# Performance work log

Measured on AMD Instinct MI355X. Metric: run time of the kernel, lower is better.

## Reference

```python
import jax, jax.numpy as jnp
import numpy as np

D_MODEL = 1024
NUM_HEADS = 16

def setup_inputs() -> dict:
    key = jax.random.key(0)
    ks = jax.random.split(key, 5)
    std = np.sqrt(2.0 / (D_MODEL + D_MODEL))
    def w(k):
        # trunc_normal approx: normal clipped to +-3 std
        v = jax.random.truncated_normal(k, -3.0, 3.0, (D_MODEL, D_MODEL), dtype=jnp.float32) * std
        return v
    return {
        "x": jax.random.normal(ks[0], (2, 2048, D_MODEL), dtype=jnp.float32),
        "w_q": w(ks[1]),
        "w_k": w(ks[2]),
        "w_v": w(ks[3]),
        "w_o": w(ks[4]),
    }

def reference(x, w_q, w_k, w_v, w_o):
    B, S, D = x.shape
    H = NUM_HEADS
    dk = D // H
    # Linear: y = x @ W^T  (weight is [d_out, d_in])
    def proj(w):
        y = jnp.einsum('bsd,ed->bse', x, w)
        return y.reshape(B, S, H, dk).transpose(0, 2, 1, 3)  # [B,H,S,dk]
    q, k, v = proj(w_q), proj(w_k), proj(w_v)
    scale = 1.0 / jnp.sqrt(jnp.float32(dk))
    scores = jnp.einsum('bhqd,bhkd->bhqk', q, k) * scale  # [B,H,S,S]
    causal = jnp.tril(jnp.ones((S, S), dtype=bool))
    scores = jnp.where(causal, scores, -jnp.inf)
    attn = jax.nn.softmax(scores, axis=-1)
    out = jnp.einsum('bhqk,bhkd->bhqd', attn, v)  # [B,H,S,dk]
    out = out.transpose(0, 2, 1, 3).reshape(B, S, D)
    return jnp.einsum('bsd,ed->bse', out, w_o)
```

## Files before the change

### kernel.cpp

```cpp
#include <hip/hip_runtime.h>
#include <hip/hip_bf16.h>
#include <stdint.h>

#define S_LEN 2048
#define DM    1024
#define NH    16
#define DK    64
#define NBATCH 2

typedef __attribute__((ext_vector_type(8))) short bf8_t;
typedef __attribute__((ext_vector_type(4))) short s4_t;
typedef __attribute__((ext_vector_type(4))) float f4_t;

using bf16 = __hip_bfloat16;

#define NEG_BIG (-1.0e30f)
#define SCALE2  (0.125f * 1.44269504088896f)

static __device__ __forceinline__ f4_t mfma16(bf8_t a, bf8_t b, f4_t c) {
    return __builtin_amdgcn_mfma_f32_16x16x32_bf16(a, b, c, 0, 0, 0);
}

static __device__ __forceinline__ short f2b(float f) {
    __hip_bfloat16 h = __float2bfloat16(f);
    return *reinterpret_cast<short*>(&h);
}

__global__ __launch_bounds__(256)
void gemm_qkv(const float* __restrict__ x,
              const float* __restrict__ wqp, const float* __restrict__ wkp,
              const float* __restrict__ wvp,
              bf16* __restrict__ qws, bf16* __restrict__ kws,
              bf16* __restrict__ vtws) {
    constexpr int K = DM;
    constexpr int BM = 128, BK = 32, LDT = BK + 8;

    const int z = blockIdx.z;
    const float* W = (z == 0) ? wqp : (z == 1) ? wkp : wvp;

    __shared__ bf16 As[BM][LDT];
    __shared__ bf16 Bs[BM][LDT];

    const int tid  = threadIdx.x;
    const int lane = tid & 63;
    const int w    = tid >> 6;
    const int wr   = w >> 1, wc = w & 1;
    const int lhi  = lane >> 4, llo = lane & 15;
    const int bm   = blockIdx.x * BM;
    const int bn   = blockIdx.y * BM;

    f4_t acc[4][4] = {};

    for (int k0 = 0; k0 < K; k0 += BK) {
        __syncthreads();
        #pragma unroll
        for (int t = 0; t < 2; ++t) {
            int c   = t * 256 + tid;
            int row = c >> 2;
            int col = (c & 3) << 3;
            {
                const float* s0 = x + (size_t)(bm + row) * K + k0 + col;
                float4 f0 = *(const float4*)(s0);
                float4 f1 = *(const float4*)(s0 + 4);
                bf8_t a8;
                a8[0]=f2b(f0.x); a8[1]=f2b(f0.y); a8[2]=f2b(f0.z); a8[3]=f2b(f0.w);
                a8[4]=f2b(f1.x); a8[5]=f2b(f1.y); a8[6]=f2b(f1.z); a8[7]=f2b(f1.w);
                *(bf8_t*)(&As[row][col]) = a8;
            }
            {
                const float* s0 = W + (size_t)(bn + row) * K + k0 + col;
                float4 f0 = *(const float4*)(s0);
                float4 f1 = *(const float4*)(s0 + 4);
                bf8_t b8;
                b8[0]=f2b(f0.x); b8[1]=f2b(f0.y); b8[2]=f2b(f0.z); b8[3]=f2b(f0.w);
                b8[4]=f2b(f1.x); b8[5]=f2b(f1.y); b8[6]=f2b(f1.z); b8[7]=f2b(f1.w);
                *(bf8_t*)(&Bs[row][col]) = b8;
            }
        }
        __syncthreads();

        bf8_t af[4], bfr[4];
        #pragma unroll
        for (int i = 0; i < 4; ++i) {
            af[i]  = *(const bf8_t*)(&As[wr * 64 + i * 16 + llo][lhi * 8]);
            bfr[i] = *(const bf8_t*)(&Bs[wc * 64 + i * 16 + llo][lhi * 8]);
        }
        #pragma unroll
        for (int mi = 0; mi < 4; ++mi)
            #pragma unroll
            for (int ni = 0; ni < 4; ++ni)
                acc[mi][ni] = mfma16(af[mi], bfr[ni], acc[mi][ni]);
    }

    if (z < 2) {
        bf16* C = z ? kws : qws;
        const float sc = z ? 1.0f : SCALE2;
        #pragma unroll
        for (int mi = 0; mi < 4; ++mi)
            #pragma unroll
            for (int ni = 0; ni < 4; ++ni)
                #pragma unroll
                for (int r = 0; r < 4; ++r) {
                    int m = bm + wr * 64 + mi * 16 + lhi * 4 + r;
                    int n = bn + wc * 64 + ni * 16 + llo;
                    int b = m >> 11, s = m & (S_LEN - 1);
                    int h = n >> 6,  d = n & (DK - 1);
                    C[(((size_t)(b * NH + h) * S_LEN) + s) * DK + d] =
                        __float2bfloat16(acc[mi][ni][r] * sc);
                }
    } else {
        #pragma unroll
        for (int mi = 0; mi < 4; ++mi)
            #pragma unroll
            for (int ni = 0; ni < 4; ++ni) {
                int m0 = bm + wr * 64 + mi * 16 + lhi * 4;
                int n  = bn + wc * 64 + ni * 16 + llo;
                int b = m0 >> 11, s0 = m0 & (S_LEN - 1);
                int h = n >> 6,   d  = n & (DK - 1);
                s4_t pk;
                #pragma unroll
                for (int r = 0; r < 4; ++r) pk[r] = f2b(acc[mi][ni][r]);
                *(s4_t*)&vtws[(((size_t)(b * NH + h) * DK) + d) * S_LEN + s0] = pk;
            }
    }
}

__global__ __launch_bounds__(256)
void gemm_o(const bf16* __restrict__ A, const float* __restrict__ W,
            float* __restrict__ C) {
    constexpr int N = DM;
    constexpr int K = DM;
    constexpr int BM = 128, BN = 64, BK = 32, LDT = BK + 8;

    __shared__ bf16 As[BM][LDT];
    __shared__ bf16 Bs[BN][LDT];

    const int tid  = threadIdx.x;
    const int lane = tid & 63;
    const int w    = tid >> 6;
    const int wr   = w >> 1, wc = w & 1;
    const int lhi  = lane >> 4, llo = lane & 15;
    const int bm   = blockIdx.x * BM;
    const int bn   = blockIdx.y * BN;

    f4_t acc[4][2] = {};

    for (int k0 = 0; k0 < K; k0 += BK) {
        __syncthreads();
        #pragma unroll
        for (int t = 0; t < 2; ++t) {
            int c   = t * 256 + tid;
            int row = c >> 2;
            int col = (c & 3) << 3;
            *(bf8_t*)(&As[row][col]) =
                *(const bf8_t*)(A + (size_t)(bm + row) * K + k0 + col);
        }
        {
            int row = tid >> 2;
            int col = (tid & 3) << 3;
            const float* s0 = W + (size_t)(bn + row) * K + k0 + col;
            float4 f0 = *(const float4*)(s0);
            float4 f1 = *(const float4*)(s0 + 4);
            bf8_t b8;
            b8[0]=f2b(f0.x); b8[1]=f2b(f0.y); b8[2]=f2b(f0.z); b8[3]=f2b(f0.w);
            b8[4]=f2b(f1.x); b8[5]=f2b(f1.y); b8[6]=f2b(f1.z); b8[7]=f2b(f1.w);
            *(bf8_t*)(&Bs[row][col]) = b8;
        }
        __syncthreads();

        bf8_t af[4], bfr[2];
        #pragma unroll
        for (int i = 0; i < 4; ++i)
            af[i] = *(const bf8_t*)(&As[wr * 64 + i * 16 + llo][lhi * 8]);
        #pragma unroll
        for (int i = 0; i < 2; ++i)
            bfr[i] = *(const bf8_t*)(&Bs[wc * 32 + i * 16 + llo][lhi * 8]);
        #pragma unroll
        for (int mi = 0; mi < 4; ++mi)
            #pragma unroll
            for (int ni = 0; ni < 2; ++ni)
                acc[mi][ni] = mfma16(af[mi], bfr[ni], acc[mi][ni]);
    }

    #pragma unroll
    for (int mi = 0; mi < 4; ++mi)
        #pragma unroll
        for (int ni = 0; ni < 2; ++ni)
            #pragma unroll
            for (int r = 0; r < 4; ++r) {
                int m = bm + wr * 64 + mi * 16 + lhi * 4 + r;
                int n = bn + wc * 32 + ni * 16 + llo;
                C[(size_t)m * N + n] = acc[mi][ni][r];
            }
}

__global__ __launch_bounds__(256, 3)
void attn_fwd(const bf16* __restrict__ Q, const bf16* __restrict__ K,
              const bf16* __restrict__ Vt, bf16* __restrict__ AO) {
    __shared__ bf16 Ks[2][64][72];
    __shared__ bf16 Vs[2][64][72];
    __shared__ bf16 Pl[4][16][72];

    const int bh = blockIdx.x;
    const int qt = 31 - (int)blockIdx.y;
    const int q0 = qt * 64;
    const int nt = qt + 1;

    const bf16* Qh = Q  + (size_t)bh * S_LEN * DK;
    const bf16* Kh = K  + (size_t)bh * S_LEN * DK;
    const bf16* Vh = Vt + (size_t)bh * DK * S_LEN;

    const int tid  = threadIdx.x;
    const int lane = tid & 63;
    const int w    = tid >> 6;
    const int lhi  = lane >> 4, llo = lane & 15;
    const int r0   = tid >> 3;
    const int scol = (tid & 7) << 3;

    const bf16* qrow = Qh + (size_t)(q0 + w * 16 + llo) * DK;
    const bf8_t qf0 = *(const bf8_t*)(qrow + lhi * 8);
    const bf8_t qf1 = *(const bf8_t*)(qrow + 32 + lhi * 8);

    bf8_t ones;
    #pragma unroll
    for (int j = 0; j < 8; ++j) ones[j] = (short)0x3F80;

    *(bf8_t*)&Ks[0][r0][scol]      = *(const bf8_t*)(Kh + (size_t)r0 * DK + scol);
    *(bf8_t*)&Ks[0][r0 + 32][scol] = *(const bf8_t*)(Kh + (size_t)(r0 + 32) * DK + scol);
    *(bf8_t*)&Vs[0][r0][scol]      = *(const bf8_t*)(Vh + (size_t)r0 * S_LEN + scol);
    *(bf8_t*)&Vs[0][r0 + 32][scol] = *(const bf8_t*)(Vh + (size_t)(r0 + 32) * S_LEN + scol);
    __syncthreads();

    f4_t o[4] = {};
    float lr[4] = {0.f, 0.f, 0.f, 0.f};
    float mr = NEG_BIG;

    bf8_t kr0, kr1, vr0, vr1;

    for (int t = 0; t < nt; ++t) {
        const int kv0 = t * 64;
        const int cur = t & 1;

        if (t + 1 < nt) {
            kr0 = *(const bf8_t*)(Kh + (size_t)(kv0 + 64 + r0) * DK + scol);
            kr1 = *(const bf8_t*)(Kh + (size_t)(kv0 + 96 + r0) * DK + scol);
            vr0 = *(const bf8_t*)(Vh + (size_t)r0 * S_LEN + kv0 + 64 + scol);
            vr1 = *(const bf8_t*)(Vh + (size_t)(r0 + 32) * S_LEN + kv0 + 64 + scol);
        }

        f4_t s[4] = {};
        __builtin_amdgcn_s_setprio(1);
        #pragma unroll
        for (int nf = 0; nf < 4; ++nf) {
            bf8_t k0f = *(const bf8_t*)&Ks[cur][nf * 16 + llo][lhi * 8];
            bf8_t k1f = *(const bf8_t*)&Ks[cur][nf * 16 + llo][32 + lhi * 8];
            s[nf] = mfma16(k0f, qf0, s[nf]);
            s[nf] = mfma16(k1f, qf1, s[nf]);
        }
        __builtin_amdgcn_s_setprio(0);

        if (kv0 == q0) {
            const int qloc = w * 16 + llo;
            #pragma unroll
            for (int nf = 0; nf < 4; ++nf)
                #pragma unroll
                for (int r = 0; r < 4; ++r)
                    if (nf * 16 + lhi * 4 + r > qloc) s[nf][r] = NEG_BIG;
        }

        float pm = s[0][0];
        #pragma unroll
        for (int nf = 0; nf < 4; ++nf)
            #pragma unroll
            for (int r = 0; r < 4; ++r) pm = fmaxf(pm, s[nf][r]);
        pm = fmaxf(pm, __shfl_xor(pm, 16));
        pm = fmaxf(pm, __shfl_xor(pm, 32));

        float mn = fmaxf(mr, pm);
        float alpha = exp2f(mr - mn);
        mr = mn;

        #pragma unroll
        for (int nf = 0; nf < 4; ++nf) {
            s4_t pk;
            #pragma unroll
            for (int r = 0; r < 4; ++r) pk[r] = f2b(exp2f(s[nf][r] - mr));
            *(s4_t*)&Pl[w][llo][nf * 16 + lhi * 4] = pk;
        }

        float alpha_o[4];
        #pragma unroll
        for (int r = 0; r < 4; ++r) alpha_o[r] = __shfl(alpha, lhi * 4 + r);
        #pragma unroll
        for (int df = 0; df < 4; ++df)
            #pragma unroll
            for (int r = 0; r < 4; ++r) o[df][r] *= alpha_o[r];

        asm volatile("s_waitcnt lgkmcnt(0)" ::: "memory");
        __builtin_amdgcn_sched_barrier(0);

        bf8_t pa0 = *(const bf8_t*)&Pl[w][llo][lhi * 8];
        bf8_t pa1 = *(const bf8_t*)&Pl[w][llo][32 + lhi * 8];

        f4_t rsacc = {};
        rsacc = mfma16(pa0, ones, rsacc);
        rsacc = mfma16(pa1, ones, rsacc);

        __builtin_amdgcn_s_setprio(1);
        #pragma unroll
        for (int df = 0; df < 4; ++df) {
            bf8_t vb0 = *(const bf8_t*)&Vs[cur][df * 16 + llo][lhi * 8];
            bf8_t vb1 = *(const bf8_t*)&Vs[cur][df * 16 + llo][32 + lhi * 8];
            o[df] = mfma16(pa0, vb0, o[df]);
            o[df] = mfma16(pa1, vb1, o[df]);
        }
        __builtin_amdgcn_s_setprio(0);

        #pragma unroll
        for (int r = 0; r < 4; ++r) lr[r] = lr[r] * alpha_o[r] + rsacc[r];

        if (t + 1 < nt) {
            *(bf8_t*)&Ks[cur ^ 1][r0][scol]      = kr0;
            *(bf8_t*)&Ks[cur ^ 1][r0 + 32][scol] = kr1;
            *(bf8_t*)&Vs[cur ^ 1][r0][scol]      = vr0;
            *(bf8_t*)&Vs[cur ^ 1][r0 + 32][scol] = vr1;
        }
        __syncthreads();
    }

    const int b = bh >> 4, h = bh & (NH - 1);
    #pragma unroll
    for (int r = 0; r < 4; ++r) {
        float inv = 1.0f / lr[r];
        int q = q0 + w * 16 + lhi * 4 + r;
        bf16* orow = AO + ((size_t)(b * S_LEN + q) * DM) + h * DK;
        #pragma unroll
        for (int df = 0; df < 4; ++df)
            orow[df * 16 + llo] = __float2bfloat16(o[df][r] * inv);
    }
}

extern "C" void kernel_launch(void* const* d_in, const int* in_sizes, int n_in,
                              void* d_out, int out_size, void* d_ws, size_t ws_size,
                              hipStream_t stream) {
    const float* x  = (const float*)d_in[0];
    const float* wq = (const float*)d_in[1];
    const float* wk = (const float*)d_in[2];
    const float* wv = (const float*)d_in[3];
    const float* wo = (const float*)d_in[4];
    float* out = (float*)d_out;

    const size_t elems = (size_t)NBATCH * S_LEN * DM;
    if (ws_size < elems * 4 * sizeof(bf16)) return;

    bf16* qws  = (bf16*)d_ws;
    bf16* kws  = qws + elems;
    bf16* vtws = kws + elems;
    bf16* aws  = vtws + elems;

    dim3 blk(256);
    gemm_qkv<<<dim3(32, 8, 3), blk, 0, stream>>>(x, wq, wk, wv, qws, kws, vtws);
    attn_fwd<<<dim3(NBATCH * NH, 32), blk, 0, stream>>>(qws, kws, vtws, aws);
    gemm_o<<<dim3(32, 16), blk, 0, stream>>>(aws, wo, out);
}
```

Measured before the change: 124.6 us.

## Pre-convert inputs to bf16 and use direct global-to-LDS loads in GEMMs

```diff
diff --git a/kernel.cpp b/kernel.cpp
--- a/kernel.cpp
+++ b/kernel.cpp
@@ -26,21 +26,146 @@
     return *reinterpret_cast<short*>(&h);
 }
 
+static __device__ __forceinline__ void g2l16(const bf16* g, bf16* l) {
+#if __has_builtin(__builtin_amdgcn_global_load_lds)
+    __builtin_amdgcn_global_load_lds(
+        (const __attribute__((address_space(1))) void*)g,
+        (__attribute__((address_space(3))) void*)l, 16, 0, 0);
+#else
+    *(bf8_t*)l = *(const bf8_t*)g;
+#endif
+}
+
 __global__ __launch_bounds__(256)
-void gemm_qkv(const float* __restrict__ x,
-              const float* __restrict__ wqp, const float* __restrict__ wkp,
-              const float* __restrict__ wvp,
-              bf16* __restrict__ qws, bf16* __restrict__ kws,
-              bf16* __restrict__ vtws) {
+void cvt_all(const float* __restrict__ x,  const float* __restrict__ wq,
+             const float* __restrict__ wk, const float* __restrict__ wv,
+             const float* __restrict__ wo, bf16* __restrict__ ob) {
+    const size_t SEG = 1u << 20;
+    size_t i = ((size_t)blockIdx.x * 256 + threadIdx.x) * 8;
+    const float* src;
+    if      (i < 4 * SEG) src = x  + i;
+    else if (i < 5 * SEG) src = wq + (i - 4 * SEG);
+    else if (i < 6 * SEG) src = wk + (i - 5 * SEG);
+    else if (i < 7 * SEG) src = wv + (i - 6 * SEG);
+    else                  src = wo + (i - 7 * SEG);
+    float4 f0 = *(const float4*)(src);
+    float4 f1 = *(const float4*)(src + 4);
+    bf8_t v;
+    v[0]=f2b(f0.x); v[1]=f2b(f0.y); v[2]=f2b(f0.z); v[3]=f2b(f0.w);
+    v[4]=f2b(f1.x); v[5]=f2b(f1.y); v[6]=f2b(f1.z); v[7]=f2b(f1.w);
+    *(bf8_t*)(ob + i) = v;
+}
+
+#define GEMM_B_MAINLOOP(Aptr, Bptr)                                          \
+    __shared__ bf16 As[128][32];                                             \
+    __shared__ bf16 Bs[128][32];                                             \
+    const int tid  = threadIdx.x;                                            \
+    const int lane = tid & 63;                                               \
+    const int w    = tid >> 6;                                               \
+    const int wr   = w >> 1, wc = w & 1;                                     \
+    const int lhi  = lane >> 4, llo = lane & 15;                             \
+    const int bm   = blockIdx.x * 128;                                       \
+    const int bn   = blockIdx.y * 128;                                       \
+    const int r0c  = tid >> 2;                           \
+    const int c0c  = (tid & 3) << 3;                     \
+    const int r1c  = (256 + tid) >> 2;                                       \
+    f4_t acc[4][4] = {};                                                     \
+    for (int k0 = 0; k0 < 1024; k0 += 32) {                                  \
+        __syncthreads();                                                     \
+        g2l16(Aptr + (size_t)(bm + r0c) * 1024 + k0 + c0c,                   \
+              &As[0][0] + (size_t)tid * 8);                                  \
+        g2l16(Aptr + (size_t)(bm + r1c) * 1024 + k0 + c0c,                   \
+              &As[0][0] + (size_t)(256 + tid) * 8);                          \
+        g2l16(Bptr + (size_t)(bn + r0c) * 1024 + k0 + c0c,                   \
+              &Bs[0][0] + (size_t)tid * 8);                                  \
+        g2l16(Bptr + (size_t)(bn + r1c) * 1024 + k0 + c0c,                   \
+              &Bs[0][0] + (size_t)(256 + tid) * 8);                          \
+        asm volatile("s_waitcnt vmcnt(0)" ::: "memory");                     \
+        __syncthreads();                                                     \
+        bf8_t af[4], bfr[4];                                                 \
+        _Pragma("unroll")                                                    \
+        for (int i = 0; i < 4; ++i) {                                        \
+            af[i]  = *(const bf8_t*)(&As[wr * 64 + i * 16 + llo][lhi * 8]);  \
+            bfr[i] = *(const bf8_t*)(&Bs[wc * 64 + i * 16 + llo][lhi * 8]);  \
+        }                                                                    \
+        _Pragma("unroll")                                                    \
+        for (int mi = 0; mi < 4; ++mi)                                       \
+            _Pragma("unroll")                                                \
+            for (int ni = 0; ni < 4; ++ni)                                   \
+                acc[mi][ni] = mfma16(af[mi], bfr[ni], acc[mi][ni]);          \
+    }
+
+__global__ __launch_bounds__(256)
+void gemm_qkv_b(const bf16* __restrict__ xb,
+                const bf16* __restrict__ wqb, const bf16* __restrict__ wkb,
+                const bf16* __restrict__ wvb,
+                bf16* __restrict__ qws, bf16* __restrict__ kws,
+                bf16* __restrict__ vtws) {
+    const int z = blockIdx.z;
+    const bf16* Wb = (z == 0) ? wqb : (z == 1) ? wkb : wvb;
+    GEMM_B_MAINLOOP(xb, Wb)
+
+    if (z < 2) {
+        bf16* C = z ? kws : qws;
+        const float sc = z ? 1.0f : SCALE2;
+        #pragma unroll
+        for (int mi = 0; mi < 4; ++mi)
+            #pragma unroll
+            for (int ni = 0; ni < 4; ++ni)
+                #pragma unroll
+                for (int r = 0; r < 4; ++r) {
+                    int m = bm + wr * 64 + mi * 16 + lhi * 4 + r;
+                    int n = bn + wc * 64 + ni * 16 + llo;
+                    int b = m >> 11, s = m & (S_LEN - 1);
+                    int h = n >> 6,  d = n & (DK - 1);
+                    C[(((size_t)(b * NH + h) * S_LEN) + s) * DK + d] =
+                        __float2bfloat16(acc[mi][ni][r] * sc);
+                }
+    } else {
+        #pragma unroll
+        for (int mi = 0; mi < 4; ++mi)
+            #pragma unroll
+            for (int ni = 0; ni < 4; ++ni) {
+                int m0 = bm + wr * 64 + mi * 16 + lhi * 4;
+                int n  = bn + wc * 64 + ni * 16 + llo;
+                int b = m0 >> 11, s0 = m0 & (S_LEN - 1);
+                int h = n >> 6,   d  = n & (DK - 1);
+                s4_t pk;
+                #pragma unroll
+                for (int r = 0; r < 4; ++r) pk[r] = f2b(acc[mi][ni][r]);
+                *(s4_t*)&vtws[(((size_t)(b * NH + h) * DK) + d) * S_LEN + s0] = pk;
+            }
+    }
+}
+
+__global__ __launch_bounds__(256)
+void gemm_o_b(const bf16* __restrict__ A, const bf16* __restrict__ Wb,
+              float* __restrict__ C) {
+    GEMM_B_MAINLOOP(A, Wb)
+    #pragma unroll
+    for (int mi = 0; mi < 4; ++mi)
+        #pragma unroll
+        for (int ni = 0; ni < 4; ++ni)
+            #pragma unroll
+            for (int r = 0; r < 4; ++r) {
+                int m = bm + wr * 64 + mi * 16 + lhi * 4 + r;
+                int n = bn + wc * 64 + ni * 16 + llo;
+                C[(size_t)m * DM + n] = acc[mi][ni][r];
+            }
+}
+
+__global__ __launch_bounds__(256)
+void gemm_qkv_f32(const float* __restrict__ x,
+                  const float* __restrict__ wqp, const float* __restrict__ wkp,
+                  const float* __restrict__ wvp,
+                  bf16* __restrict__ qws, bf16* __restrict__ kws,
+                  bf16* __restrict__ vtws) {
     constexpr int K = DM;
     constexpr int BM = 128, BK = 32, LDT = BK + 8;
-
     const int z = blockIdx.z;
     const float* W = (z == 0) ? wqp : (z == 1) ? wkp : wvp;
-
     __shared__ bf16 As[BM][LDT];
     __shared__ bf16 Bs[BM][LDT];
-
     const int tid  = threadIdx.x;
     const int lane = tid & 63;
     const int w    = tid >> 6;
@@ -48,9 +173,7 @@
     const int lhi  = lane >> 4, llo = lane & 15;
     const int bm   = blockIdx.x * BM;
     const int bn   = blockIdx.y * BM;
-
     f4_t acc[4][4] = {};
-
     for (int k0 = 0; k0 < K; k0 += BK) {
         __syncthreads();
         #pragma unroll
@@ -78,7 +201,6 @@
             }
         }
         __syncthreads();
-
         bf8_t af[4], bfr[4];
         #pragma unroll
         for (int i = 0; i < 4; ++i) {
@@ -91,7 +213,6 @@
             for (int ni = 0; ni < 4; ++ni)
                 acc[mi][ni] = mfma16(af[mi], bfr[ni], acc[mi][ni]);
     }
-
     if (z < 2) {
         bf16* C = z ? kws : qws;
         const float sc = z ? 1.0f : SCALE2;
@@ -126,15 +247,13 @@
 }
 
 __global__ __launch_bounds__(256)
-void gemm_o(const bf16* __restrict__ A, const float* __restrict__ W,
-            float* __restrict__ C) {
+void gemm_o_f32(const bf16* __restrict__ A, const float* __restrict__ W,
+                float* __restrict__ C) {
     constexpr int N = DM;
     constexpr int K = DM;
     constexpr int BM = 128, BN = 64, BK = 32, LDT = BK + 8;
-
     __shared__ bf16 As[BM][LDT];
     __shared__ bf16 Bs[BN][LDT];
-
     const int tid  = threadIdx.x;
     const int lane = tid & 63;
     const int w    = tid >> 6;
@@ -142,9 +261,7 @@
     const int lhi  = lane >> 4, llo = lane & 15;
     const int bm   = blockIdx.x * BM;
     const int bn   = blockIdx.y * BN;
-
     f4_t acc[4][2] = {};
-
     for (int k0 = 0; k0 < K; k0 += BK) {
         __syncthreads();
         #pragma unroll
@@ -167,7 +284,6 @@
             *(bf8_t*)(&Bs[row][col]) = b8;
         }
         __syncthreads();
-
         bf8_t af[4], bfr[2];
         #pragma unroll
         for (int i = 0; i < 4; ++i)
@@ -181,7 +297,6 @@
             for (int ni = 0; ni < 2; ++ni)
                 acc[mi][ni] = mfma16(af[mi], bfr[ni], acc[mi][ni]);
     }
-
     #pragma unroll
     for (int mi = 0; mi < 4; ++mi)
         #pragma unroll
@@ -350,16 +465,39 @@
     const float* wo = (const float*)d_in[4];
     float* out = (float*)d_out;
 
-    const size_t elems = (size_t)NBATCH * S_LEN * DM;
-    if (ws_size < elems * 4 * sizeof(bf16)) return;
-
-    bf16* qws  = (bf16*)d_ws;
-    bf16* kws  = qws + elems;
-    bf16* vtws = kws + elems;
-    bf16* aws  = vtws + elems;
+    const size_t SEG   = 1u << 20;
+    const size_t elems = 4 * SEG;
+    const size_t need_fast = (8 * SEG + 3 * elems) * sizeof(bf16);
 
     dim3 blk(256);
-    gemm_qkv<<<dim3(32, 8, 3), blk, 0, stream>>>(x, wq, wk, wv, qws, kws, vtws);
-    attn_fwd<<<dim3(NBATCH * NH, 32), blk, 0, stream>>>(qws, kws, vtws, aws);
-    gemm_o<<<dim3(32, 16), blk, 0, stream>>>(aws, wo, out);
-}
+
+    if (ws_size >= need_fast) {
+        bf16* ob   = (bf16*)d_ws;
+        bf16* xb   = ob;
+        bf16* wqb  = ob + 4 * SEG;
+        bf16* wkb  = ob + 5 * SEG;
+        bf16* wvb  = ob + 6 * SEG;
+        bf16* wob  = ob + 7 * SEG;
+        bf16* qws  = ob + 8 * SEG;
+        bf16* kws  = qws + elems;
+        bf16* vtws = kws + elems;
+        bf16* aws  = xb;
+
+        cvt_all<<<4096, blk, 0, stream>>>(x, wq, wk, wv, wo, ob);
+        gemm_qkv_b<<<dim3(32, 8, 3), blk, 0, stream>>>(xb, wqb, wkb, wvb,
+                                                       qws, kws, vtws);
+        attn_fwd<<<dim3(NBATCH * NH, 32), blk, 0, stream>>>(qws, kws, vtws, aws);
+        gemm_o_b<<<dim3(32, 8), blk, 0, stream>>>(aws, wob, out);
+    } else {
+        if (ws_size < elems * 4 * sizeof(bf16)) return;
+        bf16* qws  = (bf16*)d_ws;
+        bf16* kws  = qws + elems;
+        bf16* vtws = kws + elems;
+        bf16* aws  = vtws + elems;
+
+        gemm_qkv_f32<<<dim3(32, 8, 3), blk, 0, stream>>>(x, wq, wk, wv,
+                                                         qws, kws, vtws);
+        attn_fwd<<<dim3(NBATCH * NH, 32), blk, 0, stream>>>(qws, kws, vtws, aws);
+        gemm_o_f32<<<dim3(32, 16), blk, 0, stream>>>(aws, wo, out);
+    }
+}
```

New measurement: 117.8 us. 5.5% less time.
